# Performance work log

Hardware: AMD Instinct MI355X
Metric: run time of the kernel (lower is better)

## Reference

```python
import jax, jax.numpy as jnp
import numpy as np

H = 256
EPS = 1e-5
WIN = (-2, -1, 1, 2)  # radius_graph(pos/2^(d+1), k=2) on unit-spaced timestamps


def leaky(x):
    return jnp.where(x >= 0, x, 0.2 * x)


def layernorm(x, g, b):
    mu = jnp.mean(x, axis=-1, keepdims=True)
    var = jnp.mean(jnp.square(x - mu), axis=-1, keepdims=True)
    return (x - mu) * jax.lax.rsqrt(var + EPS) * g + b


def nbr_mean(x, offsets):
    # mean over temporal-window neighbors within each video row; [B,T,C]
    if not offsets:
        return jnp.zeros_like(x)
    T = x.shape[1]
    idx = jnp.arange(T)
    acc = jnp.zeros_like(x)
    cnt = jnp.zeros((T,), x.dtype)
    for o in offsets:
        valid = (idx + o >= 0) & (idx + o < T)
        acc = acc + jnp.where(valid[None, :, None], jnp.roll(x, -o, axis=1), 0.0)
        cnt = cnt + valid.astype(x.dtype)
    return acc / jnp.maximum(cnt, 1.0)[None, :, None]


def conv(x, Ws, Wn, b, offsets):
    # GraphConv with mean aggregation: W_self x_i + W_nbr mean_j x_j + b
    return x @ Ws + nbr_mean(x, offsets) @ Wn + b


def stage(x, s, Wself, Wnbr, bconv, ln_g, ln_b, offsets):
    # Dropout(eval)=id; conv; LeakyReLU(0.2); conv; LayerNorm; LeakyReLU(0.2)
    x = leaky(conv(x, Wself[s, 0], Wnbr[s, 0], bconv[s, 0], offsets))
    x = conv(x, Wself[s, 1], Wnbr[s, 1], bconv[s, 1], offsets)
    return leaky(layernorm(x, ln_g[s], ln_b[s]))


def upsample2(c):
    # knn_interpolate(k=2) from coarse (stride-2 subsampled) grid back to fine grid:
    # even fine nodes coincide with a coarse node (dist 0 -> weight ~inf -> copy);
    # odd fine nodes are equidistant from two coarse nodes (0.5/0.5), except the
    # last odd node whose 2-NN are at dist s and 3s -> weights 0.9/0.1.
    even = c
    nxt = jnp.concatenate([c[:, 1:], c[:, -1:]], axis=1)
    odd = 0.5 * (c + nxt)
    odd = odd.at[:, -1].set(0.9 * c[:, -1] + 0.1 * c[:, -2])
    B, Tc, C = c.shape
    return jnp.stack([even, odd], axis=2).reshape(B, 2 * Tc, C)


def setup_inputs() -> dict:
    key = jax.random.key(0)
    ks = jax.random.split(key, 8)
    B, T, F = 16, 4096, 1024
    N = B * T
    x = jax.random.normal(ks[0], (N, 1, F), dtype=jnp.float32)
    pos = (jnp.arange(N) % T).astype(jnp.float32)
    batch = (jnp.arange(N) // T).astype(jnp.int64)
    indices = (jnp.arange(N) % T).astype(jnp.int64)
    Wp = jax.random.normal(ks[1], (F, H), dtype=jnp.float32) / np.sqrt(F)
    bp = jnp.zeros((H,), jnp.float32)
    Wself = jax.random.normal(ks[2], (6, 2, H, H), dtype=jnp.float32) / np.sqrt(H)
    Wnbr = jax.random.normal(ks[3], (6, 2, H, H), dtype=jnp.float32) / np.sqrt(H)
    bconv = jnp.zeros((6, 2, H), jnp.float32)
    ln_g = jnp.ones((6, H), jnp.float32)
    ln_b = jnp.zeros((6, H), jnp.float32)
    return {"x": x, "pos": pos, "batch": batch, "indices": indices, "B": B, "T": T,
            "Wp": Wp, "bp": bp, "Wself": Wself, "Wnbr": Wnbr, "bconv": bconv,
            "ln_g": ln_g, "ln_b": ln_b}


def reference(x, pos, batch, indices, B, T, Wp, bp, Wself, Wnbr, bconv, ln_g, ln_b):
    # input projection: Rearrange 'B S F -> B (S F)' (S=1) + Linear
    feat = x.reshape(B, T, -1) @ Wp + bp  # [B,T,H]
    # ---- Temporal Encoder ----
    f = feat
    skips = [feat]  # depth-0 input graph features
    for d in range(3):
        f = f[:, ::2]  # batch_subsampling time pooling (stride 2)
        f = f + stage(f, d, Wself, Wnbr, bconv, ln_g, ln_b, WIN)
        if d < 2:
            skips.append(f)
    # ---- Function-Aware Decoder (eval path: clustering_at_inference=False) ----
    for i in range(3):
        res = skips[2 - i]
        f = res + upsample2(f)  # knn_interpolate(k=2) + skip
        dep = 2 - i
        # radius_graph(indices, 1.5): pooled index spacing 2^dep > 1.5 for dep>=1 -> no edges
        offs = WIN if dep == 0 else ()
        f = stage(f, 3 + i, Wself, Wnbr, bconv, ln_g, ln_b, offs)
    return f  # finest-resolution decoder output [B,T,H]
```

## Files before the change

### kernel.cpp

```cpp
#include <hip/hip_runtime.h>

#define HH 256

typedef __attribute__((ext_vector_type(8))) short short8;
typedef __attribute__((ext_vector_type(4))) float f32x4;
typedef __attribute__((ext_vector_type(4))) unsigned short u16x4;
typedef __attribute__((ext_vector_type(8))) unsigned short u16x8;

constexpr int NBATCH = 16;
constexpr int T0   = 4096;
constexpr int FDIM = 1024;
constexpr int R0   = NBATCH * T0;
constexpr int R1   = R0 / 2;
constexpr int R2   = R0 / 4;
constexpr int R3   = R0 / 8;

__device__ __forceinline__ float b2f(unsigned short u) {
    union { unsigned int i; float f; } v; v.i = ((unsigned int)u) << 16; return v.f;
}
__device__ __forceinline__ unsigned short f2b(float f) {
    union { float f; unsigned int i; } v; v.f = f;
    unsigned int r = v.i + 0x7fffu + ((v.i >> 16) & 1u);
    return (unsigned short)(r >> 16);
}
__device__ __forceinline__ void gload16(const void* g, void* l) {
    __builtin_amdgcn_global_load_lds((const __attribute__((address_space(1))) void*)g,
                                     (__attribute__((address_space(3))) void*)l, 16, 0, 0);
}
__device__ __forceinline__ void barrier_sync() {
    asm volatile("s_waitcnt lgkmcnt(0)\n\ts_barrier" ::: "memory");
}
__device__ __forceinline__ void wait_vm(int n) {
    switch (n) {
    case 2: asm volatile("s_waitcnt vmcnt(2)" ::: "memory"); break;
    case 3: asm volatile("s_waitcnt vmcnt(3)" ::: "memory"); break;
    case 4: asm volatile("s_waitcnt vmcnt(4)" ::: "memory"); break;
    case 5: asm volatile("s_waitcnt vmcnt(5)" ::: "memory"); break;
    case 6: asm volatile("s_waitcnt vmcnt(6)" ::: "memory"); break;
    default: asm volatile("s_waitcnt vmcnt(0)" ::: "memory"); break;
    }
}
__device__ __forceinline__ int swz_ks(int chunk)        { return (chunk & 3) ^ ((chunk >> 3) & 3); }
__device__ __forceinline__ int frag_idx(int row, int g) { return (row * 4 + (g ^ ((row >> 1) & 3))) * 8; }

struct PVv { u16x8 v0, v1, v2, v3; };

__global__ void transpose_w(const float* __restrict__ src, unsigned short* __restrict__ dst,
                            int K, int tilesPerMat)
{
    int bid = blockIdx.x;
    int m = bid / tilesPerMat;
    int t = bid % tilesPerMat;
    int tr = t >> 3, tc = t & 7;
    const float* S = src + (size_t)m * K * HH;
    unsigned short* D = dst + (size_t)m * HH * K;
    __shared__ float tile[32][33];
    int x = threadIdx.x & 31, y = threadIdx.x >> 5;
#pragma unroll
    for (int i = y; i < 32; i += 8)
        tile[i][x] = S[(size_t)(tr * 32 + i) * HH + tc * 32 + x];
    __syncthreads();
#pragma unroll
    for (int i = y; i < 32; i += 8)
        D[(size_t)(tc * 32 + i) * K + tr * 32 + x] = f2b(tile[x][i]);
}

template<int BM, int AMODE, int NBR, int LNFUSE, int OUT>
__launch_bounds__(512)
__global__ void conv_fused(const unsigned short* __restrict__ A,
                           const unsigned short* __restrict__ Cc,
                           const unsigned short* __restrict__ prev,
                           const unsigned short* __restrict__ Bself,
                           const unsigned short* __restrict__ Bnbr,
                           const float* __restrict__ bias,
                           const float* __restrict__ lng,
                           const float* __restrict__ lnb,
                           void* __restrict__ dstv,
                           int Tl, int Tc, int tlshift)
{
    constexpr int NT = NBR ? 16 : 8;
    constexpr int MF = BM / 32;
    constexpr int WROWS = BM / 2;
    __shared__ unsigned short As[3][BM * 32];
    __shared__ unsigned short Bs[3][256 * 32];
    __shared__ float lnred[LNFUSE ? BM : 1][8];

    const int tid  = threadIdx.x;
    const int lane = tid & 63;
    const int w    = tid >> 6;
    const int wm   = w & 1, wn = w >> 1;
    const long row0 = (long)blockIdx.x * BM;

    const bool hasA   = (tid < BM * 4);
    const bool hasA_w = (w < BM / 16);
    const int arr = tid >> 2;
    const int akk = swz_ks(tid);
    const long gr = row0 + (hasA ? arr : 0);

    float ca = 0.f, cb = 0.f; size_t rc0 = 0, rc1 = 0;
    if (AMODE == 2) {
        int t = (int)(gr & (long)(Tl - 1));
        long bq = gr >> tlshift;
        int k = t >> 1;
        rc0 = (size_t)bq * Tc + k;
        if (!(t & 1))        { ca = 1.0f; cb = 0.0f; rc1 = rc0; }
        else if (k < Tc - 1) { ca = 0.5f; cb = 0.5f; rc1 = rc0 + 1; }
        else                 { ca = 0.9f; cb = 0.1f; rc1 = rc0 - 1; }
    }
    float vinv = 1.f;
    float cf0 = 0.f, cf1 = 0.f, cf2 = 0.f, cf3 = 0.f;
    size_t nrow0 = 0, nrow1 = 0, nrow2 = 0, nrow3 = 0;
    if (NBR) {
        const int offs[4] = {-2, -1, 1, 2};
        int t = (int)(gr & (long)(Tl - 1));
        int cnt = 0;
        float cf[4]; size_t nr[4];
#pragma unroll
        for (int oi = 0; oi < 4; oi++) {
            int tn = t + offs[oi];
            bool v = (tn >= 0 && tn < Tl);
            cnt += v ? 1 : 0;
            int tcl = tn < 0 ? 0 : (tn > Tl - 1 ? Tl - 1 : tn);
            long r = gr - t + tcl;
            nr[oi] = (size_t)((AMODE == 1) ? 2 * r : r) * HH;
            cf[oi] = v ? 1.f : 0.f;
        }
        vinv = 1.f / (float)cnt;
        cf0 = cf[0]; cf1 = cf[1]; cf2 = cf[2]; cf3 = cf[3];
        nrow0 = nr[0]; nrow1 = nr[1]; nrow2 = nr[2]; nrow3 = nr[3];
    }

    f32x4 acc[MF][4] = {};
    PVv pvE = {}, pvO = {};

    auto Lof = [&](int t) -> int {
        if (!hasA_w) return 2;
        const int seg = (NBR && t >= 8) ? 1 : 0;
        return seg ? 6 : (AMODE == 2 ? 5 : 3);
    };
    auto issueB = [&](int t) {
        const int seg = (NBR && t >= 8) ? 1 : 0;
        const int k0 = (t & 7) * 32;
        const int sl = t % 3;
        const unsigned short* __restrict__ Bm = seg ? Bnbr : Bself;
        gload16(Bm + (size_t)arr * HH + k0 + akk * 8,         &Bs[sl][tid * 8]);
        gload16(Bm + (size_t)(128 + arr) * HH + k0 + akk * 8, &Bs[sl][(tid + 512) * 8]);
    };
    auto issueA = [&](int t, PVv& pv) {
        if (!hasA) return;
        const int seg = (NBR && t >= 8) ? 1 : 0;
        const int k0 = (t & 7) * 32;
        const int sl = t % 3;
        if (seg == 0) {
            if (AMODE == 0) {
                gload16(A + (size_t)gr * HH + k0 + akk * 8, &As[sl][tid * 8]);
            } else if (AMODE == 1) {
                gload16(A + (size_t)(2 * gr) * HH + k0 + akk * 8, &As[sl][tid * 8]);
            } else {
                pv.v0 = *(const u16x8*)(A + (size_t)gr * HH + k0 + akk * 8);
                pv.v1 = *(const u16x8*)(Cc + rc0 * HH + k0 + akk * 8);
                pv.v2 = *(const u16x8*)(Cc + rc1 * HH + k0 + akk * 8);
            }
        } else {
            pv.v0 = *(const u16x8*)(A + nrow0 + k0 + akk * 8);
            pv.v1 = *(const u16x8*)(A + nrow1 + k0 + akk * 8);
            pv.v2 = *(const u16x8*)(A + nrow2 + k0 + akk * 8);
            pv.v3 = *(const u16x8*)(A + nrow3 + k0 + akk * 8);
        }
    };
    auto finishA = [&](int t, PVv& pv) {
        if (!hasA) return;
        const int seg = (NBR && t >= 8) ? 1 : 0;
        const int sl = t % 3;
        if (seg == 0) {
            if (AMODE == 2) {
                u16x8 o;
#pragma unroll
                for (int j = 0; j < 8; j++)
                    o[j] = f2b(b2f(pv.v0[j]) + ca * b2f(pv.v1[j]) + cb * b2f(pv.v2[j]));
                *(u16x8*)&As[sl][tid * 8] = o;
            }
        } else {
            u16x8 o;
#pragma unroll
            for (int j = 0; j < 8; j++) {
                float a = cf0 * b2f(pv.v0[j]) + cf1 * b2f(pv.v1[j])
                        + cf2 * b2f(pv.v2[j]) + cf3 * b2f(pv.v3[j]);
                o[j] = f2b(a * vinv);
            }
            *(u16x8*)&As[sl][tid * 8] = o;
        }
    };

    issueB(0); issueA(0, pvE);
    issueB(1); issueA(1, pvO);
    wait_vm(Lof(1));
    finishA(0, pvE);
    barrier_sync();

#pragma unroll
    for (int t = 0; t < NT; ++t) {
        if (t + 2 < NT) {
            issueB(t + 2);
            if (((t + 2) & 1) == 0) issueA(t + 2, pvE); else issueA(t + 2, pvO);
        }

        const int sl = t % 3;
        __builtin_amdgcn_s_setprio(1);
        short8 af[MF], bg[4];
#pragma unroll
        for (int i = 0; i < MF; i++)
            af[i] = *(const short8*)&As[sl][frag_idx(wm * WROWS + i * 16 + (lane & 15), lane >> 4)];
#pragma unroll
        for (int i = 0; i < 4; i++)
            bg[i] = *(const short8*)&Bs[sl][frag_idx(wn * 64 + i * 16 + (lane & 15), lane >> 4)];
#pragma unroll
        for (int mi = 0; mi < MF; mi++)
#pragma unroll
            for (int ni = 0; ni < 4; ni++)
                acc[mi][ni] = __builtin_amdgcn_mfma_f32_16x16x32_bf16(af[mi], bg[ni], acc[mi][ni], 0, 0, 0);
        __builtin_amdgcn_s_setprio(0);

        if (t + 1 < NT) {
            wait_vm((t + 2 < NT) ? Lof(t + 2) : 0);
            if (((t + 1) & 1) == 0) finishA(t + 1, pvE); else finishA(t + 1, pvO);
            barrier_sync();
        }
    }

    if (LNFUSE == 0) {
        unsigned short* outp = (unsigned short*)dstv;
#pragma unroll
        for (int mi = 0; mi < MF; mi++) {
            size_t rbase = (size_t)row0 + wm * WROWS + mi * 16 + (lane >> 4) * 4;
#pragma unroll
            for (int ni = 0; ni < 4; ni++) {
                int c = wn * 64 + ni * 16 + (lane & 15);
                float bb = bias[c];
                f32x4 v = acc[mi][ni];
#pragma unroll
                for (int r = 0; r < 4; r++) {
                    float t = v[r] + bb;
                    t = (t >= 0.f) ? t : 0.2f * t;
                    outp[(rbase + r) * HH + c] = f2b(t);
                }
            }
        }
    } else {
        float bb[4];
#pragma unroll
        for (int ni = 0; ni < 4; ni++) bb[ni] = bias[wn * 64 + ni * 16 + (lane & 15)];

#pragma unroll
        for (int mi = 0; mi < MF; mi++) {
#pragma unroll
            for (int r = 0; r < 4; r++) {
                float s = 0.f, q = 0.f;
#pragma unroll
                for (int ni = 0; ni < 4; ni++) {
                    float v = acc[mi][ni][r] + bb[ni];
                    s += v; q += v * v;
                }
                s += __shfl_xor(s, 1); q += __shfl_xor(q, 1);
                s += __shfl_xor(s, 2); q += __shfl_xor(q, 2);
                s += __shfl_xor(s, 4); q += __shfl_xor(q, 4);
                s += __shfl_xor(s, 8); q += __shfl_xor(q, 8);
                if ((lane & 15) == 0) {
                    int row = wm * WROWS + mi * 16 + (lane >> 4) * 4 + r;
                    lnred[row][wn]     = s;
                    lnred[row][4 + wn] = q;
                }
            }
        }
        __syncthreads();

        float gv[4], bv[4];
#pragma unroll
        for (int ni = 0; ni < 4; ni++) {
            int c = wn * 64 + ni * 16 + (lane & 15);
            gv[ni] = lng[c]; bv[ni] = lnb[c];
        }

#pragma unroll
        for (int mi = 0; mi < MF; mi++) {
#pragma unroll
            for (int r = 0; r < 4; r++) {
                int row = wm * WROWS + mi * 16 + (lane >> 4) * 4 + r;
                float s = lnred[row][0] + lnred[row][1] + lnred[row][2] + lnred[row][3];
                float q = lnred[row][4] + lnred[row][5] + lnred[row][6] + lnred[row][7];
                float mu  = s * (1.0f / HH);
                float var = q * (1.0f / HH) - mu * mu;
                float inv = rsqrtf(var + 1e-5f);
                size_t grow = (size_t)row0 + row;
#pragma unroll
                for (int ni = 0; ni < 4; ni++) {
                    int c = wn * 64 + ni * 16 + (lane & 15);
                    float v = acc[mi][ni][r] + bb[ni];
                    float y = (v - mu) * inv * gv[ni] + bv[ni];
                    y = (y >= 0.f) ? y : 0.2f * y;
                    if (OUT == 2) {
                        ((float*)dstv)[grow * HH + c] = y;
                    } else {
                        if (OUT == 1) y += b2f(prev[(2 * grow) * HH + c]);
                        ((unsigned short*)dstv)[grow * HH + c] = f2b(y);
                    }
                }
            }
        }
    }
}

__launch_bounds__(512)
__global__ void proj_gemm(const float* __restrict__ A, const unsigned short* __restrict__ Bt,
                          const float* __restrict__ bias, unsigned short* __restrict__ out)
{
    constexpr int NT = FDIM / 32;
    __shared__ unsigned short As[3][128 * 32];
    __shared__ unsigned short Bs[3][256 * 32];
    const int tid  = threadIdx.x;
    const int lane = tid & 63;
    const int w    = tid >> 6;
    const int wm   = w & 1, wn = w >> 1;
    const size_t row0 = (size_t)blockIdx.x * 128;

    const int arr = tid >> 2;
    const int akk = swz_ks(tid);

    f32x4 acc[4][4] = {};
    float4 paE0, paE1, paO0, paO1;

    auto issue = [&](int t, float4& p0, float4& p1) {
        const int k0 = t * 32;
        const int sl = t % 3;
        gload16(Bt + (size_t)arr * FDIM + k0 + akk * 8,         &Bs[sl][tid * 8]);
        gload16(Bt + (size_t)(128 + arr) * FDIM + k0 + akk * 8, &Bs[sl][(tid + 512) * 8]);
        const float* s = A + (row0 + arr) * (size_t)FDIM + k0 + akk * 8;
        p0 = *(const float4*)s;
        p1 = *(const float4*)(s + 4);
    };
    auto finish = [&](int t, float4& p0, float4& p1) {
        const int sl = t % 3;
        u16x8 o = { f2b(p0.x), f2b(p0.y), f2b(p0.z), f2b(p0.w),
                    f2b(p1.x), f2b(p1.y), f2b(p1.z), f2b(p1.w) };
        *(u16x8*)&As[sl][tid * 8] = o;
    };

    issue(0, paE0, paE1);
    issue(1, paO0, paO1);
    wait_vm(4);
    finish(0, paE0, paE1);
    barrier_sync();

#pragma unroll
    for (int t = 0; t < NT; ++t) {
        if (t + 2 < NT) {
            if (((t + 2) & 1) == 0) issue(t + 2, paE0, paE1); else issue(t + 2, paO0, paO1);
        }

        const int sl = t % 3;
        __builtin_amdgcn_s_setprio(1);
        short8 af[4], bg[4];
#pragma unroll
        for (int i = 0; i < 4; i++) {
            af[i] = *(const short8*)&As[sl][frag_idx(wm * 64 + i * 16 + (lane & 15), lane >> 4)];
            bg[i] = *(const short8*)&Bs[sl][frag_idx(wn * 64 + i * 16 + (lane & 15), lane >> 4)];
        }
#pragma unroll
        for (int mi = 0; mi < 4; mi++)
#pragma unroll
            for (int ni = 0; ni < 4; ni++)
                acc[mi][ni] = __builtin_amdgcn_mfma_f32_16x16x32_bf16(af[mi], bg[ni], acc[mi][ni], 0, 0, 0);
        __builtin_amdgcn_s_setprio(0);

        if (t + 1 < NT) {
            wait_vm((t + 2 < NT) ? 4 : 0);
            if (((t + 1) & 1) == 0) finish(t + 1, paE0, paE1); else finish(t + 1, paO0, paO1);
            barrier_sync();
        }
    }

#pragma unroll
    for (int mi = 0; mi < 4; mi++) {
        size_t rbase = row0 + wm * 64 + mi * 16 + (lane >> 4) * 4;
#pragma unroll
        for (int ni = 0; ni < 4; ni++) {
            int c = wn * 64 + ni * 16 + (lane & 15);
            float bb = bias[c];
            f32x4 v = acc[mi][ni];
#pragma unroll
            for (int r = 0; r < 4; r++)
                out[(rbase + r) * HH + c] = f2b(v[r] + bb);
        }
    }
}

__global__ void upsample_add_kernel(unsigned short* __restrict__ res, const unsigned short* __restrict__ c,
                                    int Tc, int tlshift, int Rout)
{
    int idx = blockIdx.x * 256 + threadIdx.x;
    int r = idx >> 5, cc = (idx & 31) * 8;
    if (r >= Rout) return;
    int Tl = Tc * 2;
    int t  = r & (Tl - 1);
    int bq = r >> tlshift;
    int k  = t >> 1;
    size_t rc = (size_t)bq * Tc + k;
    float u[8];
    if (!(t & 1)) {
        u16x8 v = *(const u16x8*)(c + rc * HH + cc);
#pragma unroll
        for (int j = 0; j < 8; j++) u[j] = b2f(v[j]);
    } else if (k < Tc - 1) {
        u16x8 v0 = *(const u16x8*)(c + rc * HH + cc);
        u16x8 v1 = *(const u16x8*)(c + (rc + 1) * HH + cc);
#pragma unroll
        for (int j = 0; j < 8; j++) u[j] = 0.5f * (b2f(v0[j]) + b2f(v1[j]));
    } else {
        u16x8 v0 = *(const u16x8*)(c + rc * HH + cc);
        u16x8 vm = *(const u16x8*)(c + (rc - 1) * HH + cc);
#pragma unroll
        for (int j = 0; j < 8; j++) u[j] = 0.9f * b2f(v0[j]) + 0.1f * b2f(vm[j]);
    }
    u16x8 rv = *(const u16x8*)(res + (size_t)r * HH + cc);
    u16x8 o;
#pragma unroll
    for (int j = 0; j < 8; j++) o[j] = f2b(b2f(rv[j]) + u[j]);
    *(u16x8*)(res + (size_t)r * HH + cc) = o;
}

extern "C" void kernel_launch(void* const* d_in, const int* in_sizes, int n_in,
                              void* d_out, int out_size, void* d_ws, size_t ws_size,
                              hipStream_t stream)
{
    const float* x     = (const float*)d_in[0];
    const float* Wp    = (const float*)d_in[6];
    const float* bp    = (const float*)d_in[7];
    const float* Wself = (const float*)d_in[8];
    const float* Wnbr  = (const float*)d_in[9];
    const float* bconv = (const float*)d_in[10];
    const float* ln_g  = (const float*)d_in[11];
    const float* ln_b  = (const float*)d_in[12];
    float* out = (float*)d_out;

    char* p = (char*)d_ws;
    unsigned short* Wself_t = (unsigned short*)p; p += (size_t)12 * HH * HH * 2;
    unsigned short* Wnbr_t  = (unsigned short*)p; p += (size_t)12 * HH * HH * 2;
    unsigned short* Wp_t    = (unsigned short*)p; p += (size_t)HH * FDIM * 2;
    unsigned short* c0 = (unsigned short*)p; p += (size_t)R0 * HH * 2;
    unsigned short* c1 = (unsigned short*)p; p += (size_t)R1 * HH * 2;
    unsigned short* c2 = (unsigned short*)p; p += (size_t)R2 * HH * 2;
    unsigned short* c3 = (unsigned short*)p; p += (size_t)R3 * HH * 2;
    unsigned short* t1 = (unsigned short*)p; p += (size_t)R0 * HH * 2;
    if (ws_size < (size_t)(p - (char*)d_ws)) return;

    auto Ws = [&](int i) { return Wself_t + (size_t)i * HH * HH; };
    auto Wn = [&](int i) { return Wnbr_t  + (size_t)i * HH * HH; };

    transpose_w<<<12 * 64, 256, 0, stream>>>(Wself, Wself_t, HH, 64);
    transpose_w<<<12 * 64, 256, 0, stream>>>(Wnbr,  Wnbr_t,  HH, 64);
    transpose_w<<<256, 256, 0, stream>>>(Wp, Wp_t, FDIM, 256);

    proj_gemm<<<R0 / 128, 512, 0, stream>>>(x, Wp_t, bp, c0);

    conv_fused<128, 1, 1, 0, 0><<<R1 / 128, 512, 0, stream>>>(c0, nullptr, nullptr, Ws(0), Wn(0),
        bconv + 0 * HH, nullptr, nullptr, t1, 2048, 0, 0);
    conv_fused<128, 0, 1, 1, 1><<<R1 / 128, 512, 0, stream>>>(t1, nullptr, c0, Ws(1), Wn(1),
        bconv + 1 * HH, ln_g + 0 * HH, ln_b + 0 * HH, c1, 2048, 0, 0);

    conv_fused<64, 1, 1, 0, 0><<<R2 / 64, 512, 0, stream>>>(c1, nullptr, nullptr, Ws(2), Wn(2),
        bconv + 2 * HH, nullptr, nullptr, t1, 1024, 0, 0);
    conv_fused<64, 0, 1, 1, 1><<<R2 / 64, 512, 0, stream>>>(t1, nullptr, c1, Ws(3), Wn(3),
        bconv + 3 * HH, ln_g + 1 * HH, ln_b + 1 * HH, c2, 1024, 0, 0);

    conv_fused<64, 1, 1, 0, 0><<<R3 / 64, 512, 0, stream>>>(c2, nullptr, nullptr, Ws(4), Wn(4),
        bconv + 4 * HH, nullptr, nullptr, t1, 512, 0, 0);
    conv_fused<64, 0, 1, 1, 1><<<R3 / 64, 512, 0, stream>>>(t1, nullptr, c2, Ws(5), Wn(5),
        bconv + 5 * HH, ln_g + 2 * HH, ln_b + 2 * HH, c3, 512, 0, 0);

    conv_fused<64, 2, 0, 0, 0><<<R2 / 64, 512, 0, stream>>>(c2, c3, nullptr, Ws(6), nullptr,
        bconv + 6 * HH, nullptr, nullptr, t1, 1024, 512, 10);
    conv_fused<64, 0, 0, 1, 0><<<R2 / 64, 512, 0, stream>>>(t1, nullptr, nullptr, Ws(7), nullptr,
        bconv + 7 * HH, ln_g + 3 * HH, ln_b + 3 * HH, c2, 1024, 0, 0);

    conv_fused<128, 2, 0, 0, 0><<<R1 / 128, 512, 0, stream>>>(c1, c2, nullptr, Ws(8), nullptr,
        bconv + 8 * HH, nullptr, nullptr, t1, 2048, 1024, 11);
    conv_fused<128, 0, 0, 1, 0><<<R1 / 128, 512, 0, stream>>>(t1, nullptr, nullptr, Ws(9), nullptr,
        bconv + 9 * HH, ln_g + 4 * HH, ln_b + 4 * HH, c1, 2048, 0, 0);

    upsample_add_kernel<<<R0 / 8, 256, 0, stream>>>(c0, c1, 2048, 12, R0);
    conv_fused<128, 0, 1, 0, 0><<<R0 / 128, 512, 0, stream>>>(c0, nullptr, nullptr, Ws(10), Wn(10),
        bconv + 10 * HH, nullptr, nullptr, t1, 4096, 0, 0);
    conv_fused<128, 0, 1, 1, 2><<<R0 / 128, 512, 0, stream>>>(t1, nullptr, nullptr, Ws(11), Wn(11),
        bconv + 11 * HH, ln_g + 5 * HH, ln_b + 5 * HH, out, 4096, 0, 0);
}
```

Baseline: 363.2 us.

## Add 256-row tile conv kernel for finest-resolution decoder stage

Adds a specialized conv_fused256 kernel that processes 256 rows per block (8 waves as 4x2 with 64x128 per wave) and uses it for the two finest-resolution decoder convs. Larger tiles double weight reuse per block and halve the number of B-tile loads across the grid. Neighbor-mean rows are gathered into registers and averaged before being written to LDS. Wait counts are extended for the higher number of outstanding loads. The trade-off is more accumulator registers (128 floats per thread) and more LDS, which may lower occupancy, and the grid shrinks to 256 blocks.

```diff
diff --git a/kernel.cpp b/kernel.cpp
--- a/kernel.cpp
+++ b/kernel.cpp
@@ -32,12 +32,14 @@
 }
 __device__ __forceinline__ void wait_vm(int n) {
     switch (n) {
-    case 2: asm volatile("s_waitcnt vmcnt(2)" ::: "memory"); break;
-    case 3: asm volatile("s_waitcnt vmcnt(3)" ::: "memory"); break;
-    case 4: asm volatile("s_waitcnt vmcnt(4)" ::: "memory"); break;
-    case 5: asm volatile("s_waitcnt vmcnt(5)" ::: "memory"); break;
-    case 6: asm volatile("s_waitcnt vmcnt(6)" ::: "memory"); break;
-    default: asm volatile("s_waitcnt vmcnt(0)" ::: "memory"); break;
+    case 2:  asm volatile("s_waitcnt vmcnt(2)"  ::: "memory"); break;
+    case 3:  asm volatile("s_waitcnt vmcnt(3)"  ::: "memory"); break;
+    case 4:  asm volatile("s_waitcnt vmcnt(4)"  ::: "memory"); break;
+    case 5:  asm volatile("s_waitcnt vmcnt(5)"  ::: "memory"); break;
+    case 6:  asm volatile("s_waitcnt vmcnt(6)"  ::: "memory"); break;
+    case 8:  asm volatile("s_waitcnt vmcnt(8)"  ::: "memory"); break;
+    case 10: asm volatile("s_waitcnt vmcnt(10)" ::: "memory"); break;
+    default: asm volatile("s_waitcnt vmcnt(0)"  ::: "memory"); break;
     }
 }
 __device__ __forceinline__ int swz_ks(int chunk)        { return (chunk & 3) ^ ((chunk >> 3) & 3); }
@@ -310,6 +312,224 @@
     }
 }
 
+template<int LNFUSE, int OUT>
+__launch_bounds__(512)
+__global__ void conv_fused256(const unsigned short* __restrict__ A,
+                              const unsigned short* __restrict__ Bself,
+                              const unsigned short* __restrict__ Bnbr,
+                              const float* __restrict__ bias,
+                              const float* __restrict__ lng,
+                              const float* __restrict__ lnb,
+                              void* __restrict__ dstv,
+                              int Tl)
+{
+    constexpr int NT = 16;
+    __shared__ unsigned short As[3][256 * 32];
+    __shared__ unsigned short Bs[3][256 * 32];
+    __shared__ float lnred[LNFUSE ? 256 : 1][4];
+
+    const int tid  = threadIdx.x;
+    const int lane = tid & 63;
+    const int w    = tid >> 6;
+    const int wm   = w & 3, wn = w >> 2;
+    const long row0 = (long)blockIdx.x * 256;
+    const int arr = tid >> 2;
+    const int akk = swz_ks(tid);
+    const long gr0 = row0 + arr;
+    const long gr1 = row0 + 128 + arr;
+
+    float vinv0, vinv1;
+    float cfA[4], cfB[4];
+    unsigned int nrA[4], nrB[4];
+    {
+        const int offs[4] = {-2, -1, 1, 2};
+        int t0 = (int)(gr0 & (long)(Tl - 1));
+        int t1 = (int)(gr1 & (long)(Tl - 1));
+        int c0 = 0, c1 = 0;
+#pragma unroll
+        for (int oi = 0; oi < 4; oi++) {
+            int tn = t0 + offs[oi];
+            bool v = (tn >= 0 && tn < Tl);
+            c0 += v ? 1 : 0;
+            int tcl = tn < 0 ? 0 : (tn > Tl - 1 ? Tl - 1 : tn);
+            nrA[oi] = (unsigned int)(gr0 - t0 + tcl);
+            cfA[oi] = v ? 1.f : 0.f;
+        }
+#pragma unroll
+        for (int oi = 0; oi < 4; oi++) {
+            int tn = t1 + offs[oi];
+            bool v = (tn >= 0 && tn < Tl);
+            c1 += v ? 1 : 0;
+            int tcl = tn < 0 ? 0 : (tn > Tl - 1 ? Tl - 1 : tn);
+            nrB[oi] = (unsigned int)(gr1 - t1 + tcl);
+            cfB[oi] = v ? 1.f : 0.f;
+        }
+        vinv0 = 1.f / (float)c0;
+        vinv1 = 1.f / (float)c1;
+    }
+
+    f32x4 acc[4][8] = {};
+    u16x8 pvE[8], pvO[8];
+#pragma unroll
+    for (int i = 0; i < 8; i++) { pvE[i] = u16x8{}; pvO[i] = u16x8{}; }
+
+    auto Lof = [&](int t) -> int { return (t >= 8) ? 10 : 4; };
+    auto issueB = [&](int t) {
+        const int k0 = (t & 7) * 32;
+        const int sl = t % 3;
+        const unsigned short* __restrict__ Bm = (t >= 8) ? Bnbr : Bself;
+        gload16(Bm + (size_t)arr * HH + k0 + akk * 8,         &Bs[sl][tid * 8]);
+        gload16(Bm + (size_t)(128 + arr) * HH + k0 + akk * 8, &Bs[sl][(tid + 512) * 8]);
+    };
+    auto issueA = [&](int t, u16x8* pv) {
+        const int k0 = (t & 7) * 32;
+        const int sl = t % 3;
+        if (t < 8) {
+            gload16(A + (size_t)gr0 * HH + k0 + akk * 8, &As[sl][tid * 8]);
+            gload16(A + (size_t)gr1 * HH + k0 + akk * 8, &As[sl][(tid + 512) * 8]);
+        } else {
+#pragma unroll
+            for (int oi = 0; oi < 4; oi++)
+                pv[oi] = *(const u16x8*)(A + (size_t)nrA[oi] * HH + k0 + akk * 8);
+#pragma unroll
+            for (int oi = 0; oi < 4; oi++)
+                pv[4 + oi] = *(const u16x8*)(A + (size_t)nrB[oi] * HH + k0 + akk * 8);
+        }
+    };
+    auto finishA = [&](int t, u16x8* pv) {
+        const int sl = t % 3;
+        if (t >= 8) {
+            u16x8 o0, o1;
+#pragma unroll
+            for (int j = 0; j < 8; j++) {
+                float a = cfA[0] * b2f(pv[0][j]) + cfA[1] * b2f(pv[1][j])
+                        + cfA[2] * b2f(pv[2][j]) + cfA[3] * b2f(pv[3][j]);
+                o0[j] = f2b(a * vinv0);
+                float b = cfB[0] * b2f(pv[4][j]) + cfB[1] * b2f(pv[5][j])
+                        + cfB[2] * b2f(pv[6][j]) + cfB[3] * b2f(pv[7][j]);
+                o1[j] = f2b(b * vinv1);
+            }
+            *(u16x8*)&As[sl][tid * 8] = o0;
+            *(u16x8*)&As[sl][(tid + 512) * 8] = o1;
+        }
+    };
+
+    issueB(0); issueA(0, pvE);
+    issueB(1); issueA(1, pvO);
+    wait_vm(4);
+    finishA(0, pvE);
+    barrier_sync();
+
+#pragma unroll
+    for (int t = 0; t < NT; ++t) {
+        if (t + 2 < NT) {
+            issueB(t + 2);
+            if (((t + 2) & 1) == 0) issueA(t + 2, pvE); else issueA(t + 2, pvO);
+        }
+
+        const int sl = t % 3;
+        __builtin_amdgcn_s_setprio(1);
+        short8 af[4];
+#pragma unroll
+        for (int i = 0; i < 4; i++)
+            af[i] = *(const short8*)&As[sl][frag_idx(wm * 64 + i * 16 + (lane & 15), lane >> 4)];
+#pragma unroll
+        for (int ni = 0; ni < 8; ni++) {
+            short8 bg = *(const short8*)&Bs[sl][frag_idx(wn * 128 + ni * 16 + (lane & 15), lane >> 4)];
+#pragma unroll
+            for (int mi = 0; mi < 4; mi++)
+                acc[mi][ni] = __builtin_amdgcn_mfma_f32_16x16x32_bf16(af[mi], bg, acc[mi][ni], 0, 0, 0);
+        }
+        __builtin_amdgcn_s_setprio(0);
+
+        if (t + 1 < NT) {
+            wait_vm((t + 2 < NT) ? Lof(t + 2) : 0);
+            if (((t + 1) & 1) == 0) finishA(t + 1, pvE); else finishA(t + 1, pvO);
+            barrier_sync();
+        }
+    }
+
+    if (LNFUSE == 0) {
+        unsigned short* outp = (unsigned short*)dstv;
+#pragma unroll
+        for (int mi = 0; mi < 4; mi++) {
+            size_t rbase = (size_t)row0 + wm * 64 + mi * 16 + (lane >> 4) * 4;
+#pragma unroll
+            for (int ni = 0; ni < 8; ni++) {
+                int c = wn * 128 + ni * 16 + (lane & 15);
+                float bb = bias[c];
+                f32x4 v = acc[mi][ni];
+#pragma unroll
+                for (int r = 0; r < 4; r++) {
+                    float t = v[r] + bb;
+                    t = (t >= 0.f) ? t : 0.2f * t;
+                    outp[(rbase + r) * HH + c] = f2b(t);
+                }
+            }
+        }
+    } else {
+        float bb[8];
+#pragma unroll
+        for (int ni = 0; ni < 8; ni++) bb[ni] = bias[wn * 128 + ni * 16 + (lane & 15)];
+
+#pragma unroll
+        for (int mi = 0; mi < 4; mi++) {
+#pragma unroll
+            for (int r = 0; r < 4; r++) {
+                float s = 0.f, q = 0.f;
+#pragma unroll
+                for (int ni = 0; ni < 8; ni++) {
+                    float v = acc[mi][ni][r] + bb[ni];
+                    s += v; q += v * v;
+                }
+                s += __shfl_xor(s, 1); q += __shfl_xor(q, 1);
+                s += __shfl_xor(s, 2); q += __shfl_xor(q, 2);
+                s += __shfl_xor(s, 4); q += __shfl_xor(q, 4);
+                s += __shfl_xor(s, 8); q += __shfl_xor(q, 8);
+                if ((lane & 15) == 0) {
+                    int row = wm * 64 + mi * 16 + (lane >> 4) * 4 + r;
+                    lnred[row][wn]     = s;
+                    lnred[row][2 + wn] = q;
+                }
+            }
+        }
+        __syncthreads();
+
+        float gv[8], bv[8];
+#pragma unroll
+        for (int ni = 0; ni < 8; ni++) {
+            int c = wn * 128 + ni * 16 + (lane & 15);
+            gv[ni] = lng[c]; bv[ni] = lnb[c];
+        }
+
+#pragma unroll
+        for (int mi = 0; mi < 4; mi++) {
+#pragma unroll
+            for (int r = 0; r < 4; r++) {
+                int row = wm * 64 + mi * 16 + (lane >> 4) * 4 + r;
+                float s = lnred[row][0] + lnred[row][1];
+                float q = lnred[row][2] + lnred[row][3];
+                float mu  = s * (1.0f / HH);
+                float var = q * (1.0f / HH) - mu * mu;
+                float inv = rsqrtf(var + 1e-5f);
+                size_t grow = (size_t)row0 + row;
+#pragma unroll
+                for (int ni = 0; ni < 8; ni++) {
+                    int c = wn * 128 + ni * 16 + (lane & 15);
+                    float v = acc[mi][ni][r] + bb[ni];
+                    float y = (v - mu) * inv * gv[ni] + bv[ni];
+                    y = (y >= 0.f) ? y : 0.2f * y;
+                    if (OUT == 2) {
+                        ((float*)dstv)[grow * HH + c] = y;
+                    } else {
+                        ((unsigned short*)dstv)[grow * HH + c] = f2b(y);
+                    }
+                }
+            }
+        }
+    }
+}
+
 __launch_bounds__(512)
 __global__ void proj_gemm(const float* __restrict__ A, const unsigned short* __restrict__ Bt,
                           const float* __restrict__ bias, unsigned short* __restrict__ out)
@@ -488,8 +708,8 @@
         bconv + 9 * HH, ln_g + 4 * HH, ln_b + 4 * HH, c1, 2048, 0, 0);
 
     upsample_add_kernel<<<R0 / 8, 256, 0, stream>>>(c0, c1, 2048, 12, R0);
-    conv_fused<128, 0, 1, 0, 0><<<R0 / 128, 512, 0, stream>>>(c0, nullptr, nullptr, Ws(10), Wn(10),
-        bconv + 10 * HH, nullptr, nullptr, t1, 4096, 0, 0);
-    conv_fused<128, 0, 1, 1, 2><<<R0 / 128, 512, 0, stream>>>(t1, nullptr, nullptr, Ws(11), Wn(11),
-        bconv + 11 * HH, ln_g + 5 * HH, ln_b + 5 * HH, out, 4096, 0, 0);
-}
+    conv_fused256<0, 0><<<R0 / 256, 512, 0, stream>>>(c0, Ws(10), Wn(10),
+        bconv + 10 * HH, nullptr, nullptr, t1, 4096);
+    conv_fused256<1, 2><<<R0 / 256, 512, 0, stream>>>(t1, Ws(11), Wn(11),
+        bconv + 11 * HH, ln_g + 5 * HH, ln_b + 5 * HH, out, 4096);
+}
```

After: 402.2 us. 1.11x slower.
